# Kernel tuning notes

Measured on AMD Instinct MI355X. Metric: run time of the kernel, lower is better.

Reference implementation:

```python
import jax, jax.numpy as jnp
import numpy as np

B, L, D = 16, 1024, 768   # batch, nodes per graph, embed_dim
H, C = 4, 256             # gat_heads, gat_hidden per head
E = 8192                  # directed edges per graph (2 per triple)
NEG_SLOPE = 0.2           # PyG GATConv default negative_slope


def setup_inputs() -> dict:
    key = jax.random.key(0)
    ks = jax.random.split(key, 8)
    s = 0.02
    return {
        "text_embeddings": jax.random.normal(ks[0], (B, L, D), jnp.float32),
        "edge_index": jax.random.randint(ks[1], (B, 2, E), 0, L, jnp.int32),
        "W_gat": jax.random.normal(ks[2], (H * C, D), jnp.float32) * s,   # GATConv.lin (bias=False)
        "att_src": jax.random.normal(ks[3], (H, C), jnp.float32) * s,
        "att_dst": jax.random.normal(ks[4], (H, C), jnp.float32) * s,
        "b_gat": jnp.zeros((H * C,), jnp.float32),                        # GATConv bias (concat=True)
        "W_out": jax.random.normal(ks[5], (D, H * C + D), jnp.float32) * s,
        "b_out": jnp.zeros((D,), jnp.float32),
    }


def _gat_one(x, edge_index, W_gat, att_src, att_dst, b_gat):
    """PyG-style GATConv on one graph. x: [N,D], edge_index: [2,E] (src->dst)."""
    N = x.shape[0]
    loops = jnp.arange(N, dtype=edge_index.dtype)          # add_self_loops=True (PyG default)
    src = jnp.concatenate([edge_index[0], loops])
    dst = jnp.concatenate([edge_index[1], loops])
    h = (x @ W_gat.T).reshape(N, H, C)                     # [N,H,C]
    a_s = jnp.einsum('nhc,hc->nh', h, att_src)             # [N,H]
    a_d = jnp.einsum('nhc,hc->nh', h, att_dst)
    e = jax.nn.leaky_relu(a_s[src] + a_d[dst], NEG_SLOPE)  # [E+N,H] per-edge logits
    m = jax.ops.segment_max(e, dst, num_segments=N)        # stable softmax over each dst neighborhood
    p = jnp.exp(e - m[dst])
    denom = jax.ops.segment_sum(p, dst, num_segments=N)
    alpha = p / (denom[dst] + 1e-16)                       # [E+N,H]
    out = jax.ops.segment_sum(alpha[:, :, None] * h[src], dst, num_segments=N)  # [N,H,C]
    return out.reshape(N, H * C) + b_gat


def reference(text_embeddings, edge_index, W_gat, att_src, att_dst, b_gat, W_out, b_out):
    x_gat = jax.vmap(_gat_one, in_axes=(0, 0, None, None, None, None))(
        text_embeddings, edge_index, W_gat, att_src, att_dst, b_gat)   # [B,L,H*C]
    fused = jnp.concatenate([text_embeddings, x_gat], axis=-1)          # [B,L,D+H*C]
    return fused @ W_out.T + b_out                                      # [B,L,D]
```

## Files before the change

kernel.cpp:

```cpp
#include <hip/hip_runtime.h>
#include <hip/hip_bf16.h>

#define B_ 16
#define L_ 1024
#define D_ 768
#define H_ 4
#define C_ 256
#define E_ 8192
#define ET_ (E_ + L_)
#define HC_ (H_ * C_)
#define F_ (D_ + HC_)
#define M_ (B_ * L_)
#define NEG_SLOPE 0.2f

typedef short bf16x8 __attribute__((ext_vector_type(8)));
typedef float f32x16 __attribute__((ext_vector_type(16)));
using bf16 = __hip_bfloat16;

struct bf16x4_s { bf16 x, y, z, w; };

__device__ __forceinline__ void async_copy16(const bf16* gsrc, bf16* ldst) {
  __builtin_amdgcn_global_load_lds(
      (const __attribute__((address_space(1))) unsigned int*)gsrc,
      (__attribute__((address_space(3))) unsigned int*)ldst, 16, 0, 0);
}

#define NB_CSR 16
#define NB_X (M_ * (D_ / 8) / 256)
#define NB_W 2112
#define NB_CO 192

__global__ __launch_bounds__(256)
void prep(const float* __restrict__ x, const int* __restrict__ ei,
          const float* __restrict__ Wg, const float* __restrict__ Wout,
          const float* __restrict__ bgat, const float* __restrict__ bout,
          bf16* __restrict__ xf, bf16* __restrict__ wg_bf, bf16* __restrict__ wout_bf,
          int* __restrict__ deg_g, int* __restrict__ offs_g, int* __restrict__ csr_src,
          float* __restrict__ cout)
{
  __shared__ int s_deg[L_];
  __shared__ int s_cur[L_];
  __shared__ int s_part[256];
  const int blk = blockIdx.x;
  const int t = threadIdx.x;

  if (blk < NB_CSR) {
    const int b = blk;
    const int* srcp = ei + (long)b * 2 * E_;
    const int* dstp = srcp + E_;
    for (int i = t; i < L_; i += 256) s_deg[i] = 0;
    __syncthreads();
    for (int e = t; e < ET_; e += 256) {
      int dst = (e < E_) ? dstp[e] : (e - E_);
      atomicAdd(&s_deg[dst], 1);
    }
    __syncthreads();
    int d0 = s_deg[t*4], d1 = s_deg[t*4+1], d2 = s_deg[t*4+2], d3 = s_deg[t*4+3];
    int tsum = d0 + d1 + d2 + d3;
    s_part[t] = tsum;
    __syncthreads();
    for (int o = 1; o < 256; o <<= 1) {
      int v = (t >= o) ? s_part[t - o] : 0;
      __syncthreads();
      s_part[t] += v;
      __syncthreads();
    }
    int run = s_part[t] - tsum;
    int o0 = run, o1 = o0 + d0, o2 = o1 + d1, o3 = o2 + d2;
    s_cur[t*4] = o0; s_cur[t*4+1] = o1; s_cur[t*4+2] = o2; s_cur[t*4+3] = o3;
    int gb = b * L_ + t * 4;
    offs_g[gb] = o0; offs_g[gb+1] = o1; offs_g[gb+2] = o2; offs_g[gb+3] = o3;
    deg_g[gb] = d0; deg_g[gb+1] = d1; deg_g[gb+2] = d2; deg_g[gb+3] = d3;
    __syncthreads();
    int* csr_b = csr_src + (long)b * ET_;
    for (int e = t; e < ET_; e += 256) {
      int src = (e < E_) ? srcp[e] : (e - E_);
      int dst = (e < E_) ? dstp[e] : (e - E_);
      int slot = atomicAdd(&s_cur[dst], 1);
      csr_b[slot] = src;
    }
  } else if (blk < NB_CSR + NB_X) {
    int idx = (blk - NB_CSR) * 256 + t;
    int row = idx / (D_ / 8);
    int c8 = idx - row * (D_ / 8);
    const float4* src = (const float4*)(x + (long)row * D_ + c8 * 8);
    float4 v0 = src[0], v1 = src[1];
    bf16 o[8];
    o[0] = __float2bfloat16(v0.x); o[1] = __float2bfloat16(v0.y);
    o[2] = __float2bfloat16(v0.z); o[3] = __float2bfloat16(v0.w);
    o[4] = __float2bfloat16(v1.x); o[5] = __float2bfloat16(v1.y);
    o[6] = __float2bfloat16(v1.z); o[7] = __float2bfloat16(v1.w);
    *(uint4*)(xf + (long)row * F_ + c8 * 8) = *(const uint4*)o;
  } else if (blk < NB_CSR + NB_X + NB_W) {
    long na4 = (long)HC_ * D_ / 4;
    long nb4 = (long)D_ * F_ / 4;
    long i0 = (long)(blk - NB_CSR - NB_X) * 256 + t;
    long stride = (long)NB_W * 256;
    for (long i = i0; i < na4 + nb4; i += stride) {
      const float4 v = (i < na4) ? ((const float4*)Wg)[i] : ((const float4*)Wout)[i - na4];
      bf16x4_s o;
      o.x = __float2bfloat16(v.x);
      o.y = __float2bfloat16(v.y);
      o.z = __float2bfloat16(v.z);
      o.w = __float2bfloat16(v.w);
      if (i < na4) ((bf16x4_s*)wg_bf)[i] = o;
      else         ((bf16x4_s*)wout_bf)[i - na4] = o;
    }
  } else {
    const int lane = t & 63;
    const int wave = t >> 6;
    int o = (blk - NB_CSR - NB_X - NB_W) * 4 + wave;
    if (o < D_) {
      const float4* wrow = (const float4*)(Wout + (long)o * F_ + D_);
      const float4* bg4  = (const float4*)bgat;
      float s = 0.f;
#pragma unroll
      for (int q = 0; q < 4; q++) {
        float4 w = wrow[lane * 4 + q];
        float4 g = bg4[lane * 4 + q];
        s += w.x * g.x + w.y * g.y + w.z * g.z + w.w * g.w;
      }
#pragma unroll
      for (int sh = 1; sh < 64; sh <<= 1) s += __shfl_xor(s, sh);
      if (lane == 0) cout[o] = bout[o] + s;
    }
  }
}

#define BM 128
#define BN 128
#define BK 64

template <int OUT_BF16>
__global__ __launch_bounds__(256)
void gemm_nt_128(const bf16* __restrict__ A, int lda,
                 const bf16* __restrict__ Bm, int ldb,
                 void* __restrict__ Cm_, int ldc, int K,
                 const float* __restrict__ bias)
{
  __shared__ __align__(16) bf16 As[BM * BK];
  __shared__ __align__(16) bf16 Bs[BN * BK];
  const int t = threadIdx.x;
  const int lane = t & 63;
  const int wave = t >> 6;
  const long m0 = (long)blockIdx.x * BM;
  const long n0 = (long)blockIdx.y * BN;
  const int wm = (wave >> 1) * 64;
  const int wn = (wave & 1) * 64;
  const int lrow = lane & 31;
  const int kg = lane >> 5;

  const int sr_base = wave * 32;
  const int sr_lane = lane >> 3;
  const int c8l = lane & 7;

  f32x16 acc[2][2] = {};

  for (int k0 = 0; k0 < K; k0 += BK) {
#pragma unroll
    for (int j = 0; j < 4; j++) {
      int r = sr_base + j * 8 + sr_lane;
      int col = k0 + ((c8l ^ (r & 7)) << 3);
      bf16* ldsA = As + (sr_base + j * 8) * BK;
      bf16* ldsB = Bs + (sr_base + j * 8) * BK;
      async_copy16(A + (m0 + r) * lda + col, ldsA);
      async_copy16(Bm + (n0 + r) * ldb + col, ldsB);
    }
    __syncthreads();
#pragma unroll
    for (int ks = 0; ks < BK; ks += 16) {
      bf16x8 af[2], bfr[2];
#pragma unroll
      for (int i = 0; i < 2; i++) {
        int ra = wm + i * 32 + lrow;
        int ca = ((ks >> 3) + kg) ^ (ra & 7);
        af[i] = *(const bf16x8*)(As + ra * BK + ca * 8);
        int rb = wn + i * 32 + lrow;
        int cb = ((ks >> 3) + kg) ^ (rb & 7);
        bfr[i] = *(const bf16x8*)(Bs + rb * BK + cb * 8);
      }
#pragma unroll
      for (int i = 0; i < 2; i++)
#pragma unroll
        for (int j = 0; j < 2; j++)
          acc[i][j] = __builtin_amdgcn_mfma_f32_32x32x16_bf16(af[i], bfr[j], acc[i][j], 0, 0, 0);
    }
    __syncthreads();
  }

#pragma unroll
  for (int i = 0; i < 2; i++) {
#pragma unroll
    for (int j = 0; j < 2; j++) {
      long col = n0 + wn + j * 32 + lrow;
      float bv = bias ? bias[col] : 0.f;
#pragma unroll
      for (int reg = 0; reg < 16; reg++) {
        long row = m0 + wm + i * 32 + (reg & 3) + 8 * (reg >> 2) + 4 * kg;
        float v = acc[i][j][reg] + bv;
        if (OUT_BF16) ((bf16*)Cm_)[row * ldc + col] = __float2bfloat16(v);
        else          ((float*)Cm_)[row * ldc + col] = v;
      }
    }
  }
}

__device__ __forceinline__ void unpack16(uint4 u0, uint4 u1, float* f) {
#pragma unroll
  for (int k = 0; k < 4; k++) {
    unsigned w = ((const unsigned*)&u0)[k];
    f[2 * k]     = __uint_as_float(w << 16);
    f[2 * k + 1] = __uint_as_float(w & 0xffff0000u);
    unsigned w2 = ((const unsigned*)&u1)[k];
    f[8 + 2 * k]     = __uint_as_float(w2 << 16);
    f[8 + 2 * k + 1] = __uint_as_float(w2 & 0xffff0000u);
  }
}

__global__ __launch_bounds__(256)
void calc_asd(const bf16* __restrict__ h,
              const float* __restrict__ att_s_g, const float* __restrict__ att_d_g,
              float* __restrict__ a_s, float* __restrict__ a_d)
{
  const int t = threadIdx.x;
  const int lane = t & 63;
  const int wave = t >> 6;
  const int n = blockIdx.x * 4 + wave;
  const int c0 = lane * 16;

  float as16[16], ad16[16];
#pragma unroll
  for (int q = 0; q < 4; q++) {
    *(float4*)(as16 + 4 * q) = *(const float4*)(att_s_g + c0 + 4 * q);
    *(float4*)(ad16 + 4 * q) = *(const float4*)(att_d_g + c0 + 4 * q);
  }
  const bf16* hp = h + (long)n * HC_ + c0;
  float f[16];
  unpack16(*(const uint4*)hp, *(const uint4*)(hp + 8), f);
  float vs = 0.f, vd = 0.f;
#pragma unroll
  for (int k = 0; k < 16; k++) { vs += f[k] * as16[k]; vd += f[k] * ad16[k]; }
#pragma unroll
  for (int o = 1; o < 16; o <<= 1) { vs += __shfl_xor(vs, o); vd += __shfl_xor(vd, o); }
  if ((lane & 15) == 0) {
    int hd = lane >> 4;
    a_s[(long)n * H_ + hd] = vs;
    a_d[(long)n * H_ + hd] = vd;
  }
}

__device__ inline float lrelu(float v) { return v > 0.f ? v : NEG_SLOPE * v; }

__global__ __launch_bounds__(256)
void gat_aggregate(const int* __restrict__ offs, const int* __restrict__ deg_a,
                   const int* __restrict__ csr_src,
                   const float* __restrict__ a_s, const float* __restrict__ a_d,
                   const bf16* __restrict__ h, bf16* __restrict__ xg, int ldx)
{
  const int t = threadIdx.x;
  const int lane = t & 63;
  const int wave = t >> 6;
  const int i = blockIdx.x;
  const int b = (i & 7) + 8 * ((i >> 3) >> 8);
  const int grp = (i >> 3) & 255;
  const int bd = b * L_ + grp * 4 + wave;
  const int deg = deg_a[bd];
  const int* list = csr_src + (long)b * ET_ + offs[bd];
  const int c0 = lane * 16;
  const int hd = lane >> 4;

  const float ad = a_d[(long)bd * H_ + hd];
  const float* asb = a_s + (long)b * L_ * H_ + hd;

  float acc[16];
#pragma unroll
  for (int k = 0; k < 16; k++) acc[k] = 0.f;
  float ssum = 0.f;
  const bf16* hb = h + (long)b * L_ * HC_ + c0;

  if (deg <= 64) {
    int s_lane = (lane < deg) ? list[lane] : 0;
#pragma unroll 4
    for (int e = 0; e < deg; e++) {
      int se = __shfl(s_lane, e);
      const bf16* hp = hb + (long)se * HC_;
      uint4 u0 = *(const uint4*)hp;
      uint4 u1 = *(const uint4*)(hp + 8);
      float as = asb[(long)se * H_];
      float p = __expf(lrelu(as + ad));
      float f[16];
      unpack16(u0, u1, f);
      ssum += p;
#pragma unroll
      for (int k = 0; k < 16; k++) acc[k] += p * f[k];
    }
  } else {
    for (int e = 0; e < deg; e++) {
      int se = list[e];
      const bf16* hp = hb + (long)se * HC_;
      uint4 u0 = *(const uint4*)hp;
      uint4 u1 = *(const uint4*)(hp + 8);
      float as = asb[(long)se * H_];
      float p = __expf(lrelu(as + ad));
      float f[16];
      unpack16(u0, u1, f);
      ssum += p;
#pragma unroll
      for (int k = 0; k < 16; k++) acc[k] += p * f[k];
    }
  }

  float rs = 1.f / (ssum + 1e-16f);
  bf16 ov[16];
#pragma unroll
  for (int k = 0; k < 16; k++) ov[k] = __float2bfloat16(acc[k] * rs);
  bf16* op = xg + (long)bd * ldx + c0;
  *(uint4*)op = *(const uint4*)ov;
  *(uint4*)(op + 8) = *(const uint4*)(ov + 8);
}

extern "C" void kernel_launch(void* const* d_in, const int* in_sizes, int n_in,
                              void* d_out, int out_size, void* d_ws, size_t ws_size,
                              hipStream_t stream) {
  const float* x     = (const float*)d_in[0];
  const int*   ei    = (const int*)d_in[1];
  const float* Wg    = (const float*)d_in[2];
  const float* att_s = (const float*)d_in[3];
  const float* att_d = (const float*)d_in[4];
  const float* bgat  = (const float*)d_in[5];
  const float* Wout  = (const float*)d_in[6];
  const float* bout  = (const float*)d_in[7];
  float* out = (float*)d_out;

  char* ws = (char*)d_ws;
  size_t off = 0;
  auto alloc = [&](size_t bytes) {
    void* p = ws + off;
    off = (off + bytes + 255) & ~(size_t)255;
    return p;
  };
  bf16* xf      = (bf16*)alloc((size_t)M_ * F_ * 2);
  bf16* wg_bf   = (bf16*)alloc((size_t)HC_ * D_ * 2);
  bf16* wout_bf = (bf16*)alloc((size_t)D_ * F_ * 2);
  bf16* h_bf    = (bf16*)alloc((size_t)M_ * HC_ * 2);
  int* deg      = (int*)alloc((size_t)M_ * 4);
  int* offs     = (int*)alloc((size_t)M_ * 4);
  int* csr_src  = (int*)alloc((size_t)B_ * ET_ * 4);
  float* cout   = (float*)alloc((size_t)D_ * 4);
  float* a_s    = (float*)alloc((size_t)M_ * H_ * 4);
  float* a_d    = (float*)alloc((size_t)M_ * H_ * 4);

  prep<<<dim3(NB_CSR + NB_X + NB_W + NB_CO), dim3(256), 0, stream>>>(
      x, ei, Wg, Wout, bgat, bout, xf, wg_bf, wout_bf, deg, offs, csr_src, cout);

  gemm_nt_128<1><<<dim3(M_ / BM, HC_ / BN), dim3(256), 0, stream>>>(
      xf, F_, wg_bf, D_, h_bf, HC_, D_, nullptr);

  calc_asd<<<dim3(M_ / 4), dim3(256), 0, stream>>>(h_bf, att_s, att_d, a_s, a_d);

  gat_aggregate<<<dim3(M_ / 4), dim3(256), 0, stream>>>(offs, deg, csr_src,
                                                        a_s, a_d, h_bf, xf + D_, F_);

  gemm_nt_128<0><<<dim3(M_ / BM, D_ / BN), dim3(256), 0, stream>>>(
      xf, F_, wout_bf, F_, out, D_, F_, cout);
}
```

Measured before the change: 263.5 us.

## Fuse attention-score projection into GAT GEMM epilogue and split aggregation across waves

Removes the separate calc_asd kernel. The first GEMM's epilogue now computes per-row dot products of its fp32 accumulators with att_src and att_dst, reduces them across lanes, and atomically adds the results into a_s/a_d. Those buffers are zeroed by extra blocks in the prep kernel. The aggregation kernel also now gives each destination node two waves of 8 channels per lane instead of one wave of 16, doubling the grid for more parallelism in the gather. The cost is extra shuffles and atomics in the GEMM epilogue, and the scores are now taken from fp32 accumulators rather than bf16 h, so values differ slightly.

```diff
diff --git a/kernel.cpp b/kernel.cpp
--- a/kernel.cpp
+++ b/kernel.cpp
@@ -29,6 +29,7 @@
 #define NB_X (M_ * (D_ / 8) / 256)
 #define NB_W 2112
 #define NB_CO 192
+#define NB_Z 128
 
 __global__ __launch_bounds__(256)
 void prep(const float* __restrict__ x, const int* __restrict__ ei,
@@ -36,7 +37,7 @@
           const float* __restrict__ bgat, const float* __restrict__ bout,
           bf16* __restrict__ xf, bf16* __restrict__ wg_bf, bf16* __restrict__ wout_bf,
           int* __restrict__ deg_g, int* __restrict__ offs_g, int* __restrict__ csr_src,
-          float* __restrict__ cout)
+          float* __restrict__ cout, float* __restrict__ asd_zero)
 {
   __shared__ int s_deg[L_];
   __shared__ int s_cur[L_];
@@ -106,7 +107,7 @@
       if (i < na4) ((bf16x4_s*)wg_bf)[i] = o;
       else         ((bf16x4_s*)wout_bf)[i - na4] = o;
     }
-  } else {
+  } else if (blk < NB_CSR + NB_X + NB_W + NB_CO) {
     const int lane = t & 63;
     const int wave = t >> 6;
     int o = (blk - NB_CSR - NB_X - NB_W) * 4 + wave;
@@ -124,6 +125,9 @@
       for (int sh = 1; sh < 64; sh <<= 1) s += __shfl_xor(s, sh);
       if (lane == 0) cout[o] = bout[o] + s;
     }
+  } else {
+    int idx = (blk - NB_CSR - NB_X - NB_W - NB_CO) * 256 + t;
+    ((uint4*)asd_zero)[idx] = uint4{0u, 0u, 0u, 0u};
   }
 }
 
@@ -131,12 +135,14 @@
 #define BN 128
 #define BK 64
 
-template <int OUT_BF16>
+template <int OUT_BF16, int DO_ASD>
 __global__ __launch_bounds__(256)
 void gemm_nt_128(const bf16* __restrict__ A, int lda,
                  const bf16* __restrict__ Bm, int ldb,
                  void* __restrict__ Cm_, int ldc, int K,
-                 const float* __restrict__ bias)
+                 const float* __restrict__ bias,
+                 const float* __restrict__ att_s_g, const float* __restrict__ att_d_g,
+                 float* __restrict__ a_s, float* __restrict__ a_d)
 {
   __shared__ __align__(16) bf16 As[BM * BK];
   __shared__ __align__(16) bf16 Bs[BN * BK];
@@ -203,49 +209,41 @@
       }
     }
   }
-}
-
-__device__ __forceinline__ void unpack16(uint4 u0, uint4 u1, float* f) {
+
+  if constexpr (DO_ASD) {
+    const int hd = (int)(n0 >> 8);
+    const int cb = (int)(n0 & 255);
+    float ws[2], wd[2];
+#pragma unroll
+    for (int j = 0; j < 2; j++) {
+      int c = cb + wn + j * 32 + lrow;
+      ws[j] = att_s_g[hd * C_ + c];
+      wd[j] = att_d_g[hd * C_ + c];
+    }
+#pragma unroll
+    for (int i = 0; i < 2; i++) {
+#pragma unroll
+      for (int reg = 0; reg < 16; reg++) {
+        float ps = acc[i][0][reg] * ws[0] + acc[i][1][reg] * ws[1];
+        float pd = acc[i][0][reg] * wd[0] + acc[i][1][reg] * wd[1];
+#pragma unroll
+        for (int m = 1; m < 32; m <<= 1) { ps += __shfl_xor(ps, m); pd += __shfl_xor(pd, m); }
+        if (lrow == 0) {
+          long row = m0 + wm + i * 32 + (reg & 3) + 8 * (reg >> 2) + 4 * kg;
+          atomicAdd(a_s + row * H_ + hd, ps);
+          atomicAdd(a_d + row * H_ + hd, pd);
+        }
+      }
+    }
+  }
+}
+
+__device__ __forceinline__ void unpack8(uint4 u0, float* f) {
 #pragma unroll
   for (int k = 0; k < 4; k++) {
     unsigned w = ((const unsigned*)&u0)[k];
     f[2 * k]     = __uint_as_float(w << 16);
     f[2 * k + 1] = __uint_as_float(w & 0xffff0000u);
-    unsigned w2 = ((const unsigned*)&u1)[k];
-    f[8 + 2 * k]     = __uint_as_float(w2 << 16);
-    f[8 + 2 * k + 1] = __uint_as_float(w2 & 0xffff0000u);
-  }
-}
-
-__global__ __launch_bounds__(256)
-void calc_asd(const bf16* __restrict__ h,
-              const float* __restrict__ att_s_g, const float* __restrict__ att_d_g,
-              float* __restrict__ a_s, float* __restrict__ a_d)
-{
-  const int t = threadIdx.x;
-  const int lane = t & 63;
-  const int wave = t >> 6;
-  const int n = blockIdx.x * 4 + wave;
-  const int c0 = lane * 16;
-
-  float as16[16], ad16[16];
-#pragma unroll
-  for (int q = 0; q < 4; q++) {
-    *(float4*)(as16 + 4 * q) = *(const float4*)(att_s_g + c0 + 4 * q);
-    *(float4*)(ad16 + 4 * q) = *(const float4*)(att_d_g + c0 + 4 * q);
-  }
-  const bf16* hp = h + (long)n * HC_ + c0;
-  float f[16];
-  unpack16(*(const uint4*)hp, *(const uint4*)(hp + 8), f);
-  float vs = 0.f, vd = 0.f;
-#pragma unroll
-  for (int k = 0; k < 16; k++) { vs += f[k] * as16[k]; vd += f[k] * ad16[k]; }
-#pragma unroll
-  for (int o = 1; o < 16; o <<= 1) { vs += __shfl_xor(vs, o); vd += __shfl_xor(vd, o); }
-  if ((lane & 15) == 0) {
-    int hd = lane >> 4;
-    a_s[(long)n * H_ + hd] = vs;
-    a_d[(long)n * H_ + hd] = vd;
   }
 }
 
@@ -260,21 +258,23 @@
   const int t = threadIdx.x;
   const int lane = t & 63;
   const int wave = t >> 6;
+  const int ds = wave >> 1;
+  const int half = wave & 1;
   const int i = blockIdx.x;
-  const int b = (i & 7) + 8 * ((i >> 3) >> 8);
-  const int grp = (i >> 3) & 255;
-  const int bd = b * L_ + grp * 4 + wave;
+  const int b = (i & 7) + 8 * ((i >> 3) >> 9);
+  const int grp = (i >> 3) & 511;
+  const int bd = b * L_ + grp * 2 + ds;
   const int deg = deg_a[bd];
   const int* list = csr_src + (long)b * ET_ + offs[bd];
-  const int c0 = lane * 16;
-  const int hd = lane >> 4;
+  const int c0 = half * 512 + lane * 8;
+  const int hd = c0 >> 8;
 
   const float ad = a_d[(long)bd * H_ + hd];
   const float* asb = a_s + (long)b * L_ * H_ + hd;
 
-  float acc[16];
-#pragma unroll
-  for (int k = 0; k < 16; k++) acc[k] = 0.f;
+  float acc[8];
+#pragma unroll
+  for (int k = 0; k < 8; k++) acc[k] = 0.f;
   float ssum = 0.f;
   const bf16* hb = h + (long)b * L_ * HC_ + c0;
 
@@ -283,40 +283,35 @@
 #pragma unroll 4
     for (int e = 0; e < deg; e++) {
       int se = __shfl(s_lane, e);
-      const bf16* hp = hb + (long)se * HC_;
-      uint4 u0 = *(const uint4*)hp;
-      uint4 u1 = *(const uint4*)(hp + 8);
+      uint4 u0 = *(const uint4*)(hb + (long)se * HC_);
       float as = asb[(long)se * H_];
       float p = __expf(lrelu(as + ad));
-      float f[16];
-      unpack16(u0, u1, f);
+      float f[8];
+      unpack8(u0, f);
       ssum += p;
 #pragma unroll
-      for (int k = 0; k < 16; k++) acc[k] += p * f[k];
+      for (int k = 0; k < 8; k++) acc[k] += p * f[k];
     }
   } else {
     for (int e = 0; e < deg; e++) {
       int se = list[e];
-      const bf16* hp = hb + (long)se * HC_;
-      uint4 u0 = *(const uint4*)hp;
-      uint4 u1 = *(const uint4*)(hp + 8);
+      uint4 u0 = *(const uint4*)(hb + (long)se * HC_);
       float as = asb[(long)se * H_];
       float p = __expf(lrelu(as + ad));
-      float f[16];
-      unpack16(u0, u1, f);
+      float f[8];
+      unpack8(u0, f);
       ssum += p;
 #pragma unroll
-      for (int k = 0; k < 16; k++) acc[k] += p * f[k];
+      for (int k = 0; k < 8; k++) acc[k] += p * f[k];
     }
   }
 
   float rs = 1.f / (ssum + 1e-16f);
-  bf16 ov[16];
-#pragma unroll
-  for (int k = 0; k < 16; k++) ov[k] = __float2bfloat16(acc[k] * rs);
+  bf16 ov[8];
+#pragma unroll
+  for (int k = 0; k < 8; k++) ov[k] = __float2bfloat16(acc[k] * rs);
   bf16* op = xg + (long)bd * ldx + c0;
   *(uint4*)op = *(const uint4*)ov;
-  *(uint4*)(op + 8) = *(const uint4*)(ov + 8);
 }
 
 extern "C" void kernel_launch(void* const* d_in, const int* in_sizes, int n_in,
@@ -350,17 +345,15 @@
   float* a_s    = (float*)alloc((size_t)M_ * H_ * 4);
   float* a_d    = (float*)alloc((size_t)M_ * H_ * 4);
 
-  prep<<<dim3(NB_CSR + NB_X + NB_W + NB_CO), dim3(256), 0, stream>>>(
-      x, ei, Wg, Wout, bgat, bout, xf, wg_bf, wout_bf, deg, offs, csr_src, cout);
-
-  gemm_nt_128<1><<<dim3(M_ / BM, HC_ / BN), dim3(256), 0, stream>>>(
-      xf, F_, wg_bf, D_, h_bf, HC_, D_, nullptr);
-
-  calc_asd<<<dim3(M_ / 4), dim3(256), 0, stream>>>(h_bf, att_s, att_d, a_s, a_d);
-
-  gat_aggregate<<<dim3(M_ / 4), dim3(256), 0, stream>>>(offs, deg, csr_src,
+  prep<<<dim3(NB_CSR + NB_X + NB_W + NB_CO + NB_Z), dim3(256), 0, stream>>>(
+      x, ei, Wg, Wout, bgat, bout, xf, wg_bf, wout_bf, deg, offs, csr_src, cout, a_s);
+
+  gemm_nt_128<1, 1><<<dim3(M_ / BM, HC_ / BN), dim3(256), 0, stream>>>(
+      xf, F_, wg_bf, D_, h_bf, HC_, D_, nullptr, att_s, att_d, a_s, a_d);
+
+  gat_aggregate<<<dim3(M_ / 2), dim3(256), 0, stream>>>(offs, deg, csr_src,
                                                         a_s, a_d, h_bf, xf + D_, F_);
 
-  gemm_nt_128<0><<<dim3(M_ / BM, D_ / BN), dim3(256), 0, stream>>>(
-      xf, F_, wout_bf, F_, out, D_, F_, cout);
-}
+  gemm_nt_128<0, 0><<<dim3(M_ / BM, D_ / BN), dim3(256), 0, stream>>>(
+      xf, F_, wout_bf, F_, out, D_, F_, cout, nullptr, nullptr, nullptr, nullptr);
+}
```

New measurement: 268.9 us. +2.0%, slower.
